# Kernel tuning notes

Hardware: AMD Instinct MI355X
Metric: run time of the kernel (lower is better)

## Reference

```python
import jax, jax.numpy as jnp
import numpy as np
from jax import lax


def haar_dwt2(x):
    """Level-1 Haar (db1) 2D DWT on [N, H, W] with even H, W.
    Returns cA, cH, cV (cD is discarded by the module), each [N, H//2, W//2].
    Matches pywt/ptwt db1 block form: cA=(a+b+c+d)/2, etc."""
    a = x[:, 0::2, 0::2]
    b = x[:, 0::2, 1::2]
    c = x[:, 1::2, 0::2]
    d = x[:, 1::2, 1::2]
    cA = (a + b + c + d) * 0.5
    cH = (a + b - c - d) * 0.5  # horizontal detail (highpass along rows axis)
    cV = (a - b + c - d) * 0.5  # vertical detail (highpass along cols axis)
    return cA, cH, cV


def conv2d_same(x, w, b):
    # x: [N, Cin, H, W], w: [Cout, Cin, kh, kw]
    y = lax.conv_general_dilated(x, w, window_strides=(1, 1), padding='SAME',
                                 dimension_numbers=('NCHW', 'OIHW', 'NCHW'))
    return y + b[None, :, None, None]


def maxpool2(x):
    return lax.reduce_window(x, -jnp.inf, lax.max,
                             window_dimensions=(1, 1, 2, 2),
                             window_strides=(1, 1, 2, 2), padding='VALID')


def setup_inputs() -> dict:
    key = jax.random.key(0)
    ks = jax.random.split(key, 7)
    B, C, H, W = 32, 3, 512, 512
    x = jax.random.normal(ks[0], (B, C, H, W), dtype=jnp.float32)
    # conv stack params (Conv2d(1,16,3), Conv2d(16,8,3), Conv2d(8,4,1))
    w1 = jax.random.normal(ks[1], (16, 1, 3, 3), dtype=jnp.float32) * (1.0 / 3.0)
    b1 = jnp.zeros((16,), dtype=jnp.float32)
    w2 = jax.random.normal(ks[2], (8, 16, 3, 3), dtype=jnp.float32) * (1.0 / 12.0)
    b2 = jnp.zeros((8,), dtype=jnp.float32)
    w3 = jax.random.normal(ks[3], (4, 8, 1, 1), dtype=jnp.float32) * (1.0 / 2.83)
    b3 = jnp.zeros((4,), dtype=jnp.float32)
    return {"x": x, "w1": w1, "b1": b1, "w2": w2, "b2": b2, "w3": w3, "b3": b3}


def reference(x, w1, b1, w2, b2, w3, b3):
    B, C, H, W = x.shape
    # Batch the per-image/per-channel loop: treat each channel as one map.
    flat = x.reshape(B * C, H, W)
    cA, cH, cV = haar_dwt2(flat)  # [B*C, H/2, W/2]

    # Low-frequency conv stack on approx coeffs (1 input channel per map).
    h = cA[:, None, :, :]                       # [B*C, 1, H/2, W/2]
    h = maxpool2(jax.nn.relu(conv2d_same(h, w1, b1)))
    h = maxpool2(jax.nn.relu(conv2d_same(h, w2, b2)))
    h = conv2d_same(h, w3, b3)                  # [B*C, 4, H/8, W/8]
    # per-channel flatten, then concat over channels (dim=1 in the original)
    low = h.reshape(B, 1, -1)                   # [B, 1, C*4*(H/8)*(W/8)]

    # High-frequency: per channel concat [cH.flatten(), cV.flatten()],
    # then concat over channels.
    n = (H // 2) * (W // 2)
    high = jnp.concatenate([cH.reshape(B, C, n), cV.reshape(B, C, n)], axis=-1)
    high = high.reshape(B, 1, C * 2 * n)        # [B, 1, C*2*(H/2)*(W/2)]
    return low, high
```

## Files before the change

kernel.cpp:

```cpp
#include <hip/hip_runtime.h>


typedef float v2f __attribute__((ext_vector_type(2)));

#define PK_FMA_W0(acc, w, d) \
    asm("v_pk_fma_f32 %0, %1, %2, %0 op_sel:[0,0,0] op_sel_hi:[1,0,1]" \
        : "+v"(acc) : "s"(w), "v"(d))
#define PK_FMA_W1(acc, w, d) \
    asm("v_pk_fma_f32 %0, %1, %2, %0 op_sel:[0,1,0] op_sel_hi:[1,1,1]" \
        : "+v"(acc) : "s"(w), "v"(d))
#define PK_MUL_W0(dst, w, d) \
    asm("v_pk_mul_f32 %0, %1, %2 op_sel:[0,0] op_sel_hi:[1,0]" \
        : "=v"(dst) : "s"(w), "v"(d))
#define PK_MUL_W1(dst, w, d) \
    asm("v_pk_mul_f32 %0, %1, %2 op_sel:[0,1] op_sel_hi:[1,1]" \
        : "=v"(dst) : "s"(w), "v"(d))

__global__ __launch_bounds__(256, 8) void fused_all_kernel(
    const float* __restrict__ x,
    const float* __restrict__ w1, const float* __restrict__ b1,
    const float* __restrict__ w2, const float* __restrict__ b2,
    const float* __restrict__ w3, const float* __restrict__ b3,
    float* __restrict__ outLow, float* __restrict__ outHigh)
{
    __shared__ __align__(16) float ca[38 * 70];
    __shared__ __align__(16) float h1s[4 * 18 * 34];

    int img = blockIdx.x >> 5;
    int t   = blockIdx.x & 31;
    int tyy = t >> 2, txx = t & 3;
    int hy0 = tyy * 16 - 1, hx0 = txx * 32 - 1;
    int cy0 = tyy * 32 - 3, cx0 = txx * 64 - 3;

    const float* xi = x + img * 262144;
    float* hb = outHigh + img * 131072;

    int wvi = threadIdx.x >> 6;
    int lni = threadIdx.x & 63;

    #pragma unroll
    for (int k = 0; k < 2; ++k) {
        int i = threadIdx.x + k * 256;
        int row = i >> 4, cg = i & 15;
        int gy = tyy * 32 + row;
        int gx = txx * 64 + cg * 4;
        const float* r0 = xi + (2 * gy) * 512 + 2 * gx;
        const float* r1 = r0 + 512;
        float4 t0 = *(const float4*)(r0);
        float4 t1 = *(const float4*)(r0 + 4);
        float4 u0 = *(const float4*)(r1);
        float4 u1 = *(const float4*)(r1 + 4);
        float4 vA, vH, vV;
        vA.x = (t0.x + t0.y + u0.x + u0.y) * 0.5f;
        vH.x = (t0.x + t0.y - u0.x - u0.y) * 0.5f;
        vV.x = (t0.x - t0.y + u0.x - u0.y) * 0.5f;
        vA.y = (t0.z + t0.w + u0.z + u0.w) * 0.5f;
        vH.y = (t0.z + t0.w - u0.z - u0.w) * 0.5f;
        vV.y = (t0.z - t0.w + u0.z - u0.w) * 0.5f;
        vA.z = (t1.x + t1.y + u1.x + u1.y) * 0.5f;
        vH.z = (t1.x + t1.y - u1.x - u1.y) * 0.5f;
        vV.z = (t1.x - t1.y + u1.x - u1.y) * 0.5f;
        vA.w = (t1.z + t1.w + u1.z + u1.w) * 0.5f;
        vH.w = (t1.z + t1.w - u1.z - u1.w) * 0.5f;
        vV.w = (t1.z - t1.w + u1.z - u1.w) * 0.5f;
        int po = (gy << 8) + gx;
        *(float4*)(hb + po) = vH;
        *(float4*)(hb + 65536 + po) = vV;
        float* cp = ca + (row + 3) * 70 + cg * 4 + 3;
        cp[0] = vA.x; cp[1] = vA.y; cp[2] = vA.z; cp[3] = vA.w;
    }

    #pragma unroll
    for (int j = 0; j < 3; ++j) {
        if (j < 2 || lni < 25) {
            int i = wvi * 153 + j * 64 + lni;
            int r, c;
            if (i < 210)      { r = i / 70;              c = i - r * 70; }
            else if (i < 420) { int jj = i - 210; r = 35 + jj / 70; c = jj - (jj / 70) * 70; }
            else              { int jj = i - 420; r = 3 + jj / 6; int k6 = jj - (jj / 6) * 6;
                                c = (k6 < 3) ? k6 : (64 + k6); }
            int gy = cy0 + r, gx = cx0 + c;
            float v = 0.f;
            if ((unsigned)gy < 256u && (unsigned)gx < 256u) {
                const float* p0 = xi + (2 * gy) * 512 + 2 * gx;
                float2 a = *(const float2*)(p0);
                float2 b = *(const float2*)(p0 + 512);
                v = (a.x + a.y + b.x + b.y) * 0.5f;
            }
            ca[r * 70 + c] = v;
        }
    }

    int pos = threadIdx.x & 127;
    int ocg = __builtin_amdgcn_readfirstlane(threadIdx.x >> 7);
    int ly = pos >> 4, lx = pos & 15;

    v2f acc2[2][2][2];
    #pragma unroll
    for (int o2 = 0; o2 < 2; ++o2)
        #pragma unroll
        for (int r = 0; r < 2; ++r)
            #pragma unroll
            for (int c = 0; c < 2; ++c) acc2[o2][r][c] = (v2f){0.f, 0.f};

    __syncthreads();

    #pragma unroll 1
    for (int cc = 0; cc < 4; ++cc) {
        v2f wp1[2][9];
        #pragma unroll
        for (int o2 = 0; o2 < 2; ++o2)
            #pragma unroll
            for (int k = 0; k < 9; ++k)
                wp1[o2][k] = (v2f){ w1[(cc * 4 + o2 * 2    ) * 9 + k],
                                    w1[(cc * 4 + o2 * 2 + 1) * 9 + k] };
        if (cc) __syncthreads();

        #pragma unroll 1
        for (int j = 0; j < 3; ++j) {
            if (j < 2 || lni < 25) {
                int i = wvi * 153 + j * 64 + lni;
                int hy = i / 34, hx = i - hy * 34;
                const float* pb = ca + (2 * hy) * 70 + 2 * hx;
                v2f pr[4][2];
                #pragma unroll
                for (int r = 0; r < 4; ++r) {
                    pr[r][0] = *(const v2f*)(pb + r * 70);
                    pr[r][1] = *(const v2f*)(pb + r * 70 + 2);
                }
                bool oob = ((unsigned)(hy0 + hy) >= 128u) | ((unsigned)(hx0 + hx) >= 128u);
                v2f am[2][4];
                #pragma unroll
                for (int ky = 0; ky < 3; ++ky)
                #pragma unroll
                for (int kx = 0; kx < 3; ++kx) {
                    #pragma unroll
                    for (int o2 = 0; o2 < 2; ++o2)
                    #pragma unroll
                    for (int dy = 0; dy < 2; ++dy)
                    #pragma unroll
                    for (int dx = 0; dx < 2; ++dx) {
                        v2f d = pr[ky + dy][(kx + dx) >> 1];
                        if (ky == 0 && kx == 0) {
                            if (((kx + dx) & 1) == 0) PK_MUL_W0(am[o2][dy * 2 + dx], wp1[o2][0], d);
                            else                      PK_MUL_W1(am[o2][dy * 2 + dx], wp1[o2][0], d);
                        } else {
                            if (((kx + dx) & 1) == 0) PK_FMA_W0(am[o2][dy * 2 + dx], wp1[o2][ky * 3 + kx], d);
                            else                      PK_FMA_W1(am[o2][dy * 2 + dx], wp1[o2][ky * 3 + kx], d);
                        }
                    }
                }
                #pragma unroll
                for (int o2 = 0; o2 < 2; ++o2) {
                    float mx = fmaxf(fmaxf(am[o2][0].x, am[o2][1].x),
                                     fmaxf(am[o2][2].x, am[o2][3].x));
                    float my = fmaxf(fmaxf(am[o2][0].y, am[o2][1].y),
                                     fmaxf(am[o2][2].y, am[o2][3].y));
                    mx = fmaxf(mx + b1[cc * 4 + o2 * 2    ], 0.f);
                    my = fmaxf(my + b1[cc * 4 + o2 * 2 + 1], 0.f);
                    h1s[((o2 * 2    ) * 18 + hy) * 34 + hx] = oob ? 0.f : mx;
                    h1s[((o2 * 2 + 1) * 18 + hy) * 34 + hx] = oob ? 0.f : my;
                }
            }
        }
        __syncthreads();

        #pragma unroll
        for (int icl = 0; icl < 4; ++icl) {
            int ic = cc * 4 + icl;
            v2f wl[2][9];
            #pragma unroll
            for (int o2 = 0; o2 < 2; ++o2) {
                int oc0 = ocg * 4 + o2 * 2;
                #pragma unroll
                for (int k = 0; k < 9; ++k)
                    wl[o2][k] = (v2f){ w2[((oc0    ) * 16 + ic) * 9 + k],
                                       w2[((oc0 + 1) * 16 + ic) * 9 + k] };
            }
            const float* base = h1s + (icl * 18 + ly * 2) * 34 + lx * 2;
            v2f wr[4][2];
            #pragma unroll
            for (int r = 0; r < 4; ++r) {
                wr[r][0] = *(const v2f*)(base + r * 34);
                wr[r][1] = *(const v2f*)(base + r * 34 + 2);
            }
            #pragma unroll
            for (int ky = 0; ky < 3; ++ky)
            #pragma unroll
            for (int kx = 0; kx < 3; ++kx)
            #pragma unroll
            for (int o2 = 0; o2 < 2; ++o2) {
                #pragma unroll
                for (int r = 0; r < 2; ++r)
                #pragma unroll
                for (int c = 0; c < 2; ++c) {
                    v2f d = wr[r + ky][(c + kx) >> 1];
                    if (((c + kx) & 1) == 0) PK_FMA_W0(acc2[o2][r][c], wl[o2][ky * 3 + kx], d);
                    else                     PK_FMA_W1(acc2[o2][r][c], wl[o2][ky * 3 + kx], d);
                }
            }
        }
    }

    float h2v[4];
    #pragma unroll
    for (int o2 = 0; o2 < 2; ++o2) {
        float mx = fmaxf(fmaxf(acc2[o2][0][0].x, acc2[o2][0][1].x),
                         fmaxf(acc2[o2][1][0].x, acc2[o2][1][1].x));
        float my = fmaxf(fmaxf(acc2[o2][0][0].y, acc2[o2][0][1].y),
                         fmaxf(acc2[o2][1][0].y, acc2[o2][1][1].y));
        h2v[o2 * 2    ] = fmaxf(mx + b2[ocg * 4 + o2 * 2    ], 0.f);
        h2v[o2 * 2 + 1] = fmaxf(my + b2[ocg * 4 + o2 * 2 + 1], 0.f);
    }
    __syncthreads();
    float* hx2 = h1s;
    #pragma unroll
    for (int j = 0; j < 4; ++j) hx2[pos * 9 + ocg * 4 + j] = h2v[j];
    __syncthreads();

    float hv[8];
    #pragma unroll
    for (int ic = 0; ic < 8; ++ic) hv[ic] = hx2[pos * 9 + ic];
    float* dst = outLow + img * 16384;
    int posg = (tyy * 8 + ly) * 64 + txx * 16 + lx;
    int o3g = ocg;
    #pragma unroll
    for (int jo = 0; jo < 2; ++jo) {
        int oc3 = o3g * 2 + jo;
        float s = b3[oc3];
        #pragma unroll
        for (int ic = 0; ic < 8; ++ic) s += w3[oc3 * 8 + ic] * hv[ic];
        dst[oc3 * 4096 + posg] = s;
    }
}

extern "C" void kernel_launch(void* const* d_in, const int* in_sizes, int n_in,
                              void* d_out, int out_size, void* d_ws, size_t ws_size,
                              hipStream_t stream) {
    const float* x  = (const float*)d_in[0];
    const float* w1 = (const float*)d_in[1];
    const float* b1 = (const float*)d_in[2];
    const float* w2 = (const float*)d_in[3];
    const float* b2 = (const float*)d_in[4];
    const float* w3 = (const float*)d_in[5];
    const float* b3 = (const float*)d_in[6];
    float* out     = (float*)d_out;
    float* outLow  = out;
    float* outHigh = out + 1572864;

    fused_all_kernel<<<3072, 256, 0, stream>>>(x, w1, b1, w2, b2, w3, b3,
                                               outLow, outHigh);
}
```

Measured before the change: 208.7 us.

## Halve spatial tile height and loop each block over three tiles

```diff
diff --git a/kernel.cpp b/kernel.cpp
--- a/kernel.cpp
+++ b/kernel.cpp
@@ -23,214 +23,207 @@
     const float* __restrict__ w3, const float* __restrict__ b3,
     float* __restrict__ outLow, float* __restrict__ outHigh)
 {
-    __shared__ __align__(16) float ca[38 * 70];
-    __shared__ __align__(16) float h1s[4 * 18 * 34];
-
-    int img = blockIdx.x >> 5;
-    int t   = blockIdx.x & 31;
-    int tyy = t >> 2, txx = t & 3;
-    int hy0 = tyy * 16 - 1, hx0 = txx * 32 - 1;
-    int cy0 = tyy * 32 - 3, cx0 = txx * 64 - 3;
-
-    const float* xi = x + img * 262144;
-    float* hb = outHigh + img * 131072;
+    __shared__ __align__(16) float ca[22 * 70];
+    __shared__ __align__(16) float h1s[4 * 10 * 34];
 
     int wvi = threadIdx.x >> 6;
     int lni = threadIdx.x & 63;
 
-    #pragma unroll
-    for (int k = 0; k < 2; ++k) {
-        int i = threadIdx.x + k * 256;
-        int row = i >> 4, cg = i & 15;
-        int gy = tyy * 32 + row;
-        int gx = txx * 64 + cg * 4;
-        const float* r0 = xi + (2 * gy) * 512 + 2 * gx;
-        const float* r1 = r0 + 512;
-        float4 t0 = *(const float4*)(r0);
-        float4 t1 = *(const float4*)(r0 + 4);
-        float4 u0 = *(const float4*)(r1);
-        float4 u1 = *(const float4*)(r1 + 4);
-        float4 vA, vH, vV;
-        vA.x = (t0.x + t0.y + u0.x + u0.y) * 0.5f;
-        vH.x = (t0.x + t0.y - u0.x - u0.y) * 0.5f;
-        vV.x = (t0.x - t0.y + u0.x - u0.y) * 0.5f;
-        vA.y = (t0.z + t0.w + u0.z + u0.w) * 0.5f;
-        vH.y = (t0.z + t0.w - u0.z - u0.w) * 0.5f;
-        vV.y = (t0.z - t0.w + u0.z - u0.w) * 0.5f;
-        vA.z = (t1.x + t1.y + u1.x + u1.y) * 0.5f;
-        vH.z = (t1.x + t1.y - u1.x - u1.y) * 0.5f;
-        vV.z = (t1.x - t1.y + u1.x - u1.y) * 0.5f;
-        vA.w = (t1.z + t1.w + u1.z + u1.w) * 0.5f;
-        vH.w = (t1.z + t1.w - u1.z - u1.w) * 0.5f;
-        vV.w = (t1.z - t1.w + u1.z - u1.w) * 0.5f;
-        int po = (gy << 8) + gx;
-        *(float4*)(hb + po) = vH;
-        *(float4*)(hb + 65536 + po) = vV;
-        float* cp = ca + (row + 3) * 70 + cg * 4 + 3;
-        cp[0] = vA.x; cp[1] = vA.y; cp[2] = vA.z; cp[3] = vA.w;
-    }
-
-    #pragma unroll
-    for (int j = 0; j < 3; ++j) {
-        if (j < 2 || lni < 25) {
-            int i = wvi * 153 + j * 64 + lni;
-            int r, c;
-            if (i < 210)      { r = i / 70;              c = i - r * 70; }
-            else if (i < 420) { int jj = i - 210; r = 35 + jj / 70; c = jj - (jj / 70) * 70; }
-            else              { int jj = i - 420; r = 3 + jj / 6; int k6 = jj - (jj / 6) * 6;
-                                c = (k6 < 3) ? k6 : (64 + k6); }
-            int gy = cy0 + r, gx = cx0 + c;
-            float v = 0.f;
-            if ((unsigned)gy < 256u && (unsigned)gx < 256u) {
-                const float* p0 = xi + (2 * gy) * 512 + 2 * gx;
-                float2 a = *(const float2*)(p0);
-                float2 b = *(const float2*)(p0 + 512);
-                v = (a.x + a.y + b.x + b.y) * 0.5f;
+    int pos = threadIdx.x & 63;
+    int ocg = __builtin_amdgcn_readfirstlane(wvi);
+    int ly = pos >> 4, lx = pos & 15;
+
+    #pragma unroll 1
+    for (int j3 = 0; j3 < 3; ++j3) {
+        int tIdx = blockIdx.x * 3 + j3;
+        int img  = tIdx >> 6;
+        int s    = tIdx & 63;
+        int rs = s >> 2, cs = s & 3;
+        int hy0 = rs * 8 - 1, hx0 = cs * 32 - 1;
+        int cy0 = rs * 16 - 3, cx0 = cs * 64 - 3;
+
+        const float* xi = x + img * 262144;
+        float* hb = outHigh + img * 131072;
+
+        {
+            int i = threadIdx.x;
+            int row = i >> 4, cg = i & 15;
+            int gy = rs * 16 + row;
+            int gx = cs * 64 + cg * 4;
+            const float* r0 = xi + (2 * gy) * 512 + 2 * gx;
+            const float* r1 = r0 + 512;
+            float4 t0 = *(const float4*)(r0);
+            float4 t1 = *(const float4*)(r0 + 4);
+            float4 u0 = *(const float4*)(r1);
+            float4 u1 = *(const float4*)(r1 + 4);
+            float4 vA, vH, vV;
+            vA.x = (t0.x + t0.y + u0.x + u0.y) * 0.5f;
+            vH.x = (t0.x + t0.y - u0.x - u0.y) * 0.5f;
+            vV.x = (t0.x - t0.y + u0.x - u0.y) * 0.5f;
+            vA.y = (t0.z + t0.w + u0.z + u0.w) * 0.5f;
+            vH.y = (t0.z + t0.w - u0.z - u0.w) * 0.5f;
+            vV.y = (t0.z - t0.w + u0.z - u0.w) * 0.5f;
+            vA.z = (t1.x + t1.y + u1.x + u1.y) * 0.5f;
+            vH.z = (t1.x + t1.y - u1.x - u1.y) * 0.5f;
+            vV.z = (t1.x - t1.y + u1.x - u1.y) * 0.5f;
+            vA.w = (t1.z + t1.w + u1.z + u1.w) * 0.5f;
+            vH.w = (t1.z + t1.w - u1.z - u1.w) * 0.5f;
+            vV.w = (t1.z - t1.w + u1.z - u1.w) * 0.5f;
+            int po = (gy << 8) + gx;
+            *(float4*)(hb + po) = vH;
+            *(float4*)(hb + 65536 + po) = vV;
+            float* cp = ca + (row + 3) * 70 + cg * 4 + 3;
+            cp[0] = vA.x; cp[1] = vA.y; cp[2] = vA.z; cp[3] = vA.w;
+        }
+
+        #pragma unroll
+        for (int j = 0; j < 3; ++j) {
+            if (j < 2 || lni < 1) {
+                int i = wvi * 129 + j * 64 + lni;
+                int r, c;
+                if (i < 210)      { r = i / 70;              c = i - r * 70; }
+                else if (i < 420) { int jj = i - 210; r = 19 + jj / 70; c = jj - (jj / 70) * 70; }
+                else              { int jj = i - 420; r = 3 + jj / 6; int k6 = jj - (jj / 6) * 6;
+                                    c = (k6 < 3) ? k6 : (64 + k6); }
+                int gy = cy0 + r, gx = cx0 + c;
+                float v = 0.f;
+                if ((unsigned)gy < 256u && (unsigned)gx < 256u) {
+                    const float* p0 = xi + (2 * gy) * 512 + 2 * gx;
+                    float2 a = *(const float2*)(p0);
+                    float2 b = *(const float2*)(p0 + 512);
+                    v = (a.x + a.y + b.x + b.y) * 0.5f;
+                }
+                ca[r * 70 + c] = v;
             }
-            ca[r * 70 + c] = v;
-        }
-    }
-
-    int pos = threadIdx.x & 127;
-    int ocg = __builtin_amdgcn_readfirstlane(threadIdx.x >> 7);
-    int ly = pos >> 4, lx = pos & 15;
-
-    v2f acc2[2][2][2];
-    #pragma unroll
-    for (int o2 = 0; o2 < 2; ++o2)
+        }
+
+        v2f acc2[2][2];
         #pragma unroll
         for (int r = 0; r < 2; ++r)
             #pragma unroll
-            for (int c = 0; c < 2; ++c) acc2[o2][r][c] = (v2f){0.f, 0.f};
-
-    __syncthreads();
-
-    #pragma unroll 1
-    for (int cc = 0; cc < 4; ++cc) {
-        v2f wp1[2][9];
-        #pragma unroll
-        for (int o2 = 0; o2 < 2; ++o2)
+            for (int c = 0; c < 2; ++c) acc2[r][c] = (v2f){0.f, 0.f};
+
+        __syncthreads();
+
+        #pragma unroll 1
+        for (int cc = 0; cc < 4; ++cc) {
+            v2f wp1[2][9];
             #pragma unroll
-            for (int k = 0; k < 9; ++k)
-                wp1[o2][k] = (v2f){ w1[(cc * 4 + o2 * 2    ) * 9 + k],
-                                    w1[(cc * 4 + o2 * 2 + 1) * 9 + k] };
-        if (cc) __syncthreads();
-
-        #pragma unroll 1
-        for (int j = 0; j < 3; ++j) {
-            if (j < 2 || lni < 25) {
-                int i = wvi * 153 + j * 64 + lni;
-                int hy = i / 34, hx = i - hy * 34;
-                const float* pb = ca + (2 * hy) * 70 + 2 * hx;
-                v2f pr[4][2];
+            for (int o2 = 0; o2 < 2; ++o2)
+                #pragma unroll
+                for (int k = 0; k < 9; ++k)
+                    wp1[o2][k] = (v2f){ w1[(cc * 4 + o2 * 2    ) * 9 + k],
+                                        w1[(cc * 4 + o2 * 2 + 1) * 9 + k] };
+            if (cc) __syncthreads();
+
+            #pragma unroll 1
+            for (int j = 0; j < 2; ++j) {
+                if (j < 1 || lni < 21) {
+                    int i = wvi * 85 + j * 64 + lni;
+                    int hy = i / 34, hx = i - hy * 34;
+                    const float* pb = ca + (2 * hy) * 70 + 2 * hx;
+                    v2f pr[4][2];
+                    #pragma unroll
+                    for (int r = 0; r < 4; ++r) {
+                        pr[r][0] = *(const v2f*)(pb + r * 70);
+                        pr[r][1] = *(const v2f*)(pb + r * 70 + 2);
+                    }
+                    bool oob = ((unsigned)(hy0 + hy) >= 128u) | ((unsigned)(hx0 + hx) >= 128u);
+                    v2f am[2][4];
+                    #pragma unroll
+                    for (int ky = 0; ky < 3; ++ky)
+                    #pragma unroll
+                    for (int kx = 0; kx < 3; ++kx) {
+                        #pragma unroll
+                        for (int o2 = 0; o2 < 2; ++o2)
+                        #pragma unroll
+                        for (int dy = 0; dy < 2; ++dy)
+                        #pragma unroll
+                        for (int dx = 0; dx < 2; ++dx) {
+                            v2f d = pr[ky + dy][(kx + dx) >> 1];
+                            if (ky == 0 && kx == 0) {
+                                if (((kx + dx) & 1) == 0) PK_MUL_W0(am[o2][dy * 2 + dx], wp1[o2][0], d);
+                                else                      PK_MUL_W1(am[o2][dy * 2 + dx], wp1[o2][0], d);
+                            } else {
+                                if (((kx + dx) & 1) == 0) PK_FMA_W0(am[o2][dy * 2 + dx], wp1[o2][ky * 3 + kx], d);
+                                else                      PK_FMA_W1(am[o2][dy * 2 + dx], wp1[o2][ky * 3 + kx], d);
+                            }
+                        }
+                    }
+                    #pragma unroll
+                    for (int o2 = 0; o2 < 2; ++o2) {
+                        float mx = fmaxf(fmaxf(am[o2][0].x, am[o2][1].x),
+                                         fmaxf(am[o2][2].x, am[o2][3].x));
+                        float my = fmaxf(fmaxf(am[o2][0].y, am[o2][1].y),
+                                         fmaxf(am[o2][2].y, am[o2][3].y));
+                        mx = fmaxf(mx + b1[cc * 4 + o2 * 2    ], 0.f);
+                        my = fmaxf(my + b1[cc * 4 + o2 * 2 + 1], 0.f);
+                        h1s[((o2 * 2    ) * 10 + hy) * 34 + hx] = oob ? 0.f : mx;
+                        h1s[((o2 * 2 + 1) * 10 + hy) * 34 + hx] = oob ? 0.f : my;
+                    }
+                }
+            }
+            __syncthreads();
+
+            #pragma unroll
+            for (int icl = 0; icl < 4; ++icl) {
+                int ic = cc * 4 + icl;
+                v2f wl[9];
+                {
+                    int oc0 = ocg * 2;
+                    #pragma unroll
+                    for (int k = 0; k < 9; ++k)
+                        wl[k] = (v2f){ w2[((oc0    ) * 16 + ic) * 9 + k],
+                                       w2[((oc0 + 1) * 16 + ic) * 9 + k] };
+                }
+                const float* base = h1s + (icl * 10 + ly * 2) * 34 + lx * 2;
+                v2f wr[4][2];
                 #pragma unroll
                 for (int r = 0; r < 4; ++r) {
-                    pr[r][0] = *(const v2f*)(pb + r * 70);
-                    pr[r][1] = *(const v2f*)(pb + r * 70 + 2);
-                }
-                bool oob = ((unsigned)(hy0 + hy) >= 128u) | ((unsigned)(hx0 + hx) >= 128u);
-                v2f am[2][4];
+                    wr[r][0] = *(const v2f*)(base + r * 34);
+                    wr[r][1] = *(const v2f*)(base + r * 34 + 2);
+                }
                 #pragma unroll
                 for (int ky = 0; ky < 3; ++ky)
                 #pragma unroll
                 for (int kx = 0; kx < 3; ++kx) {
                     #pragma unroll
-                    for (int o2 = 0; o2 < 2; ++o2)
-                    #pragma unroll
-                    for (int dy = 0; dy < 2; ++dy)
-                    #pragma unroll
-                    for (int dx = 0; dx < 2; ++dx) {
-                        v2f d = pr[ky + dy][(kx + dx) >> 1];
-                        if (ky == 0 && kx == 0) {
-                            if (((kx + dx) & 1) == 0) PK_MUL_W0(am[o2][dy * 2 + dx], wp1[o2][0], d);
-                            else                      PK_MUL_W1(am[o2][dy * 2 + dx], wp1[o2][0], d);
-                        } else {
-                            if (((kx + dx) & 1) == 0) PK_FMA_W0(am[o2][dy * 2 + dx], wp1[o2][ky * 3 + kx], d);
-                            else                      PK_FMA_W1(am[o2][dy * 2 + dx], wp1[o2][ky * 3 + kx], d);
-                        }
-                    }
-                }
-                #pragma unroll
-                for (int o2 = 0; o2 < 2; ++o2) {
-                    float mx = fmaxf(fmaxf(am[o2][0].x, am[o2][1].x),
-                                     fmaxf(am[o2][2].x, am[o2][3].x));
-                    float my = fmaxf(fmaxf(am[o2][0].y, am[o2][1].y),
-                                     fmaxf(am[o2][2].y, am[o2][3].y));
-                    mx = fmaxf(mx + b1[cc * 4 + o2 * 2    ], 0.f);
-                    my = fmaxf(my + b1[cc * 4 + o2 * 2 + 1], 0.f);
-                    h1s[((o2 * 2    ) * 18 + hy) * 34 + hx] = oob ? 0.f : mx;
-                    h1s[((o2 * 2 + 1) * 18 + hy) * 34 + hx] = oob ? 0.f : my;
+                    for (int r = 0; r < 2; ++r)
+                    #pragma unroll
+                    for (int c = 0; c < 2; ++c) {
+                        v2f d = wr[r + ky][(c + kx) >> 1];
+                        if (((c + kx) & 1) == 0) PK_FMA_W0(acc2[r][c], wl[ky * 3 + kx], d);
+                        else                     PK_FMA_W1(acc2[r][c], wl[ky * 3 + kx], d);
+                    }
                 }
             }
         }
+
+        float h2a, h2b;
+        {
+            float mx = fmaxf(fmaxf(acc2[0][0].x, acc2[0][1].x),
+                             fmaxf(acc2[1][0].x, acc2[1][1].x));
+            float my = fmaxf(fmaxf(acc2[0][0].y, acc2[0][1].y),
+                             fmaxf(acc2[1][0].y, acc2[1][1].y));
+            h2a = fmaxf(mx + b2[ocg * 2    ], 0.f);
+            h2b = fmaxf(my + b2[ocg * 2 + 1], 0.f);
+        }
         __syncthreads();
-
-        #pragma unroll
-        for (int icl = 0; icl < 4; ++icl) {
-            int ic = cc * 4 + icl;
-            v2f wl[2][9];
-            #pragma unroll
-            for (int o2 = 0; o2 < 2; ++o2) {
-                int oc0 = ocg * 4 + o2 * 2;
-                #pragma unroll
-                for (int k = 0; k < 9; ++k)
-                    wl[o2][k] = (v2f){ w2[((oc0    ) * 16 + ic) * 9 + k],
-                                       w2[((oc0 + 1) * 16 + ic) * 9 + k] };
-            }
-            const float* base = h1s + (icl * 18 + ly * 2) * 34 + lx * 2;
-            v2f wr[4][2];
-            #pragma unroll
-            for (int r = 0; r < 4; ++r) {
-                wr[r][0] = *(const v2f*)(base + r * 34);
-                wr[r][1] = *(const v2f*)(base + r * 34 + 2);
-            }
-            #pragma unroll
-            for (int ky = 0; ky < 3; ++ky)
-            #pragma unroll
-            for (int kx = 0; kx < 3; ++kx)
-            #pragma unroll
-            for (int o2 = 0; o2 < 2; ++o2) {
-                #pragma unroll
-                for (int r = 0; r < 2; ++r)
-                #pragma unroll
-                for (int c = 0; c < 2; ++c) {
-                    v2f d = wr[r + ky][(c + kx) >> 1];
-                    if (((c + kx) & 1) == 0) PK_FMA_W0(acc2[o2][r][c], wl[o2][ky * 3 + kx], d);
-                    else                     PK_FMA_W1(acc2[o2][r][c], wl[o2][ky * 3 + kx], d);
-                }
-            }
-        }
-    }
-
-    float h2v[4];
-    #pragma unroll
-    for (int o2 = 0; o2 < 2; ++o2) {
-        float mx = fmaxf(fmaxf(acc2[o2][0][0].x, acc2[o2][0][1].x),
-                         fmaxf(acc2[o2][1][0].x, acc2[o2][1][1].x));
-        float my = fmaxf(fmaxf(acc2[o2][0][0].y, acc2[o2][0][1].y),
-                         fmaxf(acc2[o2][1][0].y, acc2[o2][1][1].y));
-        h2v[o2 * 2    ] = fmaxf(mx + b2[ocg * 4 + o2 * 2    ], 0.f);
-        h2v[o2 * 2 + 1] = fmaxf(my + b2[ocg * 4 + o2 * 2 + 1], 0.f);
-    }
-    __syncthreads();
-    float* hx2 = h1s;
-    #pragma unroll
-    for (int j = 0; j < 4; ++j) hx2[pos * 9 + ocg * 4 + j] = h2v[j];
-    __syncthreads();
-
-    float hv[8];
-    #pragma unroll
-    for (int ic = 0; ic < 8; ++ic) hv[ic] = hx2[pos * 9 + ic];
-    float* dst = outLow + img * 16384;
-    int posg = (tyy * 8 + ly) * 64 + txx * 16 + lx;
-    int o3g = ocg;
-    #pragma unroll
-    for (int jo = 0; jo < 2; ++jo) {
-        int oc3 = o3g * 2 + jo;
-        float s = b3[oc3];
-        #pragma unroll
-        for (int ic = 0; ic < 8; ++ic) s += w3[oc3 * 8 + ic] * hv[ic];
-        dst[oc3 * 4096 + posg] = s;
+        float* hx2 = h1s;
+        hx2[pos * 9 + ocg * 2    ] = h2a;
+        hx2[pos * 9 + ocg * 2 + 1] = h2b;
+        __syncthreads();
+
+        float hv[8];
+        #pragma unroll
+        for (int ic = 0; ic < 8; ++ic) hv[ic] = hx2[pos * 9 + ic];
+        float* dst = outLow + img * 16384;
+        int posg = (rs * 4 + ly) * 64 + cs * 16 + lx;
+        int oc3 = ocg;
+        float sacc = b3[oc3];
+        #pragma unroll
+        for (int ic = 0; ic < 8; ++ic) sacc += w3[oc3 * 8 + ic] * hv[ic];
+        dst[oc3 * 4096 + posg] = sacc;
     }
 }
 
@@ -248,6 +241,6 @@
     float* outLow  = out;
     float* outHigh = out + 1572864;
 
-    fused_all_kernel<<<3072, 256, 0, stream>>>(x, w1, b1, w2, b2, w3, b3,
+    fused_all_kernel<<<2048, 256, 0, stream>>>(x, w1, b1, w2, b2, w3, b3,
                                                outLow, outHigh);
 }
```

Result: slower. 231.4 us (+10.9%).
